# Optimization experiments

Measured on AMD Instinct MI355X. Metric: run time of the kernel, lower is better.

Reference implementation:

```python
import jax, jax.numpy as jnp
import numpy as np

B, T, FBINS = 256, 512, 128
L1, L2, L3, NCLASS = 256, 256, 128, 10
Q_SCALE = 8.0  # 4-bit fixed point in [-1, 1]


def _quant(w):
    return jnp.clip(jnp.round(w * Q_SCALE) / Q_SCALE, -1.0, 1.0)


def qw(w):
    # straight-through quantizer (identity gradient)
    return w + jax.lax.stop_gradient(_quant(w) - w)


def egru_cell(x, h, W, b, H):
    # eGRU: 2-gate cell (update gate + candidate), softsign activations
    a = jnp.concatenate([x, h], axis=-1) @ qw(W).T + b  # [B, 2H]
    z = 0.5 * (jax.nn.soft_sign(a[:, :H]) + 1.0)
    h_cand = jax.nn.soft_sign(a[:, H:])
    return z * h + (1.0 - z) * h_cand


def setup_inputs() -> dict:
    key = jax.random.key(0)
    ks = jax.random.split(key, 8)
    s = lambda fan_in: 1.0 / np.sqrt(fan_in)
    return {
        "inputs": jax.random.normal(ks[0], (B, T, FBINS), jnp.float32),
        "h1_init": jax.random.uniform(ks[1], (B, L1), jnp.float32, -1.0, 1.0),
        "h2_init": jax.random.uniform(ks[2], (B, L2), jnp.float32, -1.0, 1.0),
        "W1": jax.random.normal(ks[3], (2 * L1, FBINS + L1), jnp.float32) * s(FBINS + L1),
        "b1": jnp.zeros((2 * L1,), jnp.float32),
        "W2": jax.random.normal(ks[4], (2 * L2, L1 + L2), jnp.float32) * s(L1 + L2),
        "b2": jnp.zeros((2 * L2,), jnp.float32),
        "W3": jax.random.normal(ks[5], (L3, L2), jnp.float32) * s(L2),
        "b3": jnp.zeros((L3,), jnp.float32),
        "W4": jax.random.normal(ks[6], (NCLASS, L3), jnp.float32) * s(L3),
        "b4": jnp.zeros((NCLASS,), jnp.float32),
    }


def reference(inputs, h1_init, h2_init, W1, b1, W2, b2, W3, b3, W4, b4):
    def step(carry, x_t):
        h1, h2 = carry
        h1 = egru_cell(x_t, h1, W1, b1, L1)
        h2 = egru_cell(h1, h2, W2, b2, L2)
        h3 = jnp.maximum(h2 @ qw(W3).T + b3, 0.0)  # clamp(min=0)
        h4 = h3 @ qw(W4).T + b4
        return (h1, h2), h4

    xs = jnp.swapaxes(inputs, 0, 1)  # [T, B, F]
    _, ys = jax.lax.scan(step, (h1_init, h2_init), xs)  # [T, B, C]
    y = jnp.swapaxes(ys, 0, 1)  # [B, T, C]
    return jax.nn.log_softmax(y, axis=-1)
```

## Files before the change

### kernel.cpp

```cpp
#include <hip/hip_runtime.h>

#define NT 512
#define FB 128
#define HD 256
#define NC 10
#define NG 32
#define GR 8

typedef __attribute__((ext_vector_type(8))) short bf16x8;
typedef __attribute__((ext_vector_type(4))) float f32x4;
typedef __attribute__((ext_vector_type(4))) unsigned u32x4;

static __device__ __forceinline__ short f2bf(float f){
  union { float f; unsigned u; } v; v.f = f;
  return (short)((v.u + 0x7fffu + ((v.u >> 16) & 1u)) >> 16);
}
static __device__ __forceinline__ float bf2f(short h){
  union { unsigned u; float f; } v; v.u = ((unsigned)(unsigned short)h) << 16;
  return v.f;
}
static __device__ __forceinline__ float quantw(float w){
  return fminf(fmaxf(rintf(w * 8.0f) * 0.125f, -1.0f), 1.0f);
}
static __device__ __forceinline__ bf16x8 loadqw8(const float* __restrict__ p){
  bf16x8 v;
#pragma unroll
  for (int j = 0; j < 8; ++j) v[j] = f2bf(quantw(p[j]));
  return v;
}
static __device__ __forceinline__ void split8(f32x4 a, f32x4 b, bf16x8& hi, bf16x8& lo){
  float v0[4] = {a[0],a[1],a[2],a[3]}, v1[4] = {b[0],b[1],b[2],b[3]};
#pragma unroll
  for (int j = 0; j < 4; ++j){
    short h = f2bf(v0[j]); hi[j] = h; lo[j] = f2bf(v0[j] - bf2f(h));
  }
#pragma unroll
  for (int j = 0; j < 4; ++j){
    short h = f2bf(v1[j]); hi[4+j] = h; lo[4+j] = f2bf(v1[j] - bf2f(h));
  }
}

static __device__ __forceinline__ void st_msg(unsigned* p, short hb, short lb, unsigned ep){
  __attribute__((ext_vector_type(2))) unsigned w;
  w[0] = (((unsigned)(unsigned short)hb) << 16) | ep;
  w[1] = (((unsigned)(unsigned short)lb) << 16) | ep;
  asm volatile("global_store_dwordx2 %0, %1, off sc1" :: "v"(p), "v"(w) : "memory");
}
static __device__ __forceinline__ void gather8(const unsigned* p, unsigned ep, bf16x8& hv, bf16x8& lv){
  u32x4 a, b, c, d;
  for (;;){
    asm volatile("global_load_dwordx4 %0, %4, off sc1\n\t"
                 "global_load_dwordx4 %1, %4, off offset:16 sc1\n\t"
                 "global_load_dwordx4 %2, %4, off offset:32 sc1\n\t"
                 "global_load_dwordx4 %3, %4, off offset:48 sc1\n\t"
                 "s_waitcnt vmcnt(0)"
                 : "=&v"(a), "=&v"(b), "=&v"(c), "=&v"(d) : "v"(p) : "memory");
    unsigned m = (a[0]^ep)|(a[1]^ep)|(a[2]^ep)|(a[3]^ep)
               | (b[0]^ep)|(b[1]^ep)|(b[2]^ep)|(b[3]^ep)
               | (c[0]^ep)|(c[1]^ep)|(c[2]^ep)|(c[3]^ep)
               | (d[0]^ep)|(d[1]^ep)|(d[2]^ep)|(d[3]^ep);
    if ((m & 0xffffu) == 0u) break;
  }
  hv[0]=(short)(a[0]>>16); lv[0]=(short)(a[1]>>16);
  hv[1]=(short)(a[2]>>16); lv[1]=(short)(a[3]>>16);
  hv[2]=(short)(b[0]>>16); lv[2]=(short)(b[1]>>16);
  hv[3]=(short)(b[2]>>16); lv[3]=(short)(b[3]>>16);
  hv[4]=(short)(c[0]>>16); lv[4]=(short)(c[1]>>16);
  hv[5]=(short)(c[2]>>16); lv[5]=(short)(c[3]>>16);
  hv[6]=(short)(d[0]>>16); lv[6]=(short)(d[1]>>16);
  hv[7]=(short)(d[2]>>16); lv[7]=(short)(d[3]>>16);
}
static __device__ __forceinline__ bool chk_unpack(u32x4 a, u32x4 b, u32x4 c, u32x4 d,
                                                  unsigned ep, bf16x8& hv, bf16x8& lv){
  unsigned m = (a[0]^ep)|(a[1]^ep)|(a[2]^ep)|(a[3]^ep)
             | (b[0]^ep)|(b[1]^ep)|(b[2]^ep)|(b[3]^ep)
             | (c[0]^ep)|(c[1]^ep)|(c[2]^ep)|(c[3]^ep)
             | (d[0]^ep)|(d[1]^ep)|(d[2]^ep)|(d[3]^ep);
  if ((m & 0xffffu) != 0u) return false;
  hv[0]=(short)(a[0]>>16); lv[0]=(short)(a[1]>>16);
  hv[1]=(short)(a[2]>>16); lv[1]=(short)(a[3]>>16);
  hv[2]=(short)(b[0]>>16); lv[2]=(short)(b[1]>>16);
  hv[3]=(short)(b[2]>>16); lv[3]=(short)(b[3]>>16);
  hv[4]=(short)(c[0]>>16); lv[4]=(short)(c[1]>>16);
  hv[5]=(short)(c[2]>>16); lv[5]=(short)(c[3]>>16);
  hv[6]=(short)(d[0]>>16); lv[6]=(short)(d[1]>>16);
  hv[7]=(short)(d[2]>>16); lv[7]=(short)(d[3]>>16);
  return true;
}

#define ISSUE_G8(P,A,B,C,D) \
  asm volatile("global_load_dwordx4 %0, %4, off sc1\n\t" \
               "global_load_dwordx4 %1, %4, off offset:16 sc1\n\t" \
               "global_load_dwordx4 %2, %4, off offset:32 sc1\n\t" \
               "global_load_dwordx4 %3, %4, off offset:48 sc1" \
               : "=&v"(A),"=&v"(B),"=&v"(C),"=&v"(D) : "v"(P) : "memory")
#define ISSUE_X2(P,A,B) \
  asm volatile("global_load_dwordx4 %0, %2, off\n\t" \
               "global_load_dwordx4 %1, %2, off offset:16" \
               : "=&v"(A),"=&v"(B) : "v"(P) : "memory")
#define WAITV4(N,A,B,C,D) do{ \
  asm volatile("s_waitcnt vmcnt(" #N ")" : "+v"(A),"+v"(B),"+v"(C),"+v"(D) :: "memory"); \
  __builtin_amdgcn_sched_barrier(0); }while(0)
#define WAITV2(N,A,B) do{ \
  asm volatile("s_waitcnt vmcnt(" #N ")" : "+v"(A),"+v"(B) :: "memory"); \
  __builtin_amdgcn_sched_barrier(0); }while(0)
#define BARRIER() do{ asm volatile("s_waitcnt lgkmcnt(0)" ::: "memory"); \
  __builtin_amdgcn_s_barrier(); asm volatile("" ::: "memory"); }while(0)

__global__ __launch_bounds__(256, 1)
void egru_persistent(const float* __restrict__ xg,
                     const float* __restrict__ h1ig, const float* __restrict__ h2ig,
                     const float* __restrict__ W1g, const float* __restrict__ b1g,
                     const float* __restrict__ W2g, const float* __restrict__ b2g,
                     const float* __restrict__ W3g, const float* __restrict__ b3g,
                     const float* __restrict__ W4g, const float* __restrict__ b4g,
                     float* __restrict__ outg, float* __restrict__ wsf)
{
  const int tid = threadIdx.x;
  const int gp  = blockIdx.x & 31;
  const int sb  = blockIdx.x >> 5;
  const int wv  = tid >> 6;
  const int ln  = tid & 15;
  const int lk  = (tid >> 4) & 3;
  const int rz  = sb * 32;

  __shared__ __align__(16) short inX [16*128];
  __shared__ __align__(16) short inH1[16*256];
  __shared__ __align__(16) short inH2[16*256];
  __shared__ float aldsA[64][17];
  __shared__ float aldsB[64][17];
  __shared__ float h1own[32][GR];
  __shared__ float h2own[32][GR];
  __shared__ float h3p[128], h3q[128], h3row[128];
  __shared__ float ytmp[16];
  __shared__ float W4L[1344];
  __shared__ float b1s[64], b2s[64], b3L[128], b4L[10];

  unsigned* h1buf = reinterpret_cast<unsigned*>(wsf);
  unsigned* h2buf = h1buf + 262144;

  bf16x8 w1f[12], w2f[16], w3f[2][8];
  {
    const int arow = (wv < 2) ? (rz + wv*16 + ln) : (256 + rz + (wv-2)*16 + ln);
#pragma unroll
    for (int ks = 0; ks < 12; ++ks) w1f[ks] = loadqw8(W1g + arow*384 + ks*32 + lk*8);
#pragma unroll
    for (int ks = 0; ks < 16; ++ks) w2f[ks] = loadqw8(W2g + arow*512 + ks*32 + lk*8);
#pragma unroll
    for (int tl = 0; tl < 2; ++tl)
#pragma unroll
      for (int ks = 0; ks < 8; ++ks)
        w3f[tl][ks] = loadqw8(W3g + (wv*32 + tl*16 + ln)*256 + ks*32 + lk*8);
  }

  if (tid < 64){
    int grow = (tid < 32) ? (rz + tid) : (256 + rz + (tid - 32));
    b1s[tid] = b1g[grow];
    b2s[tid] = b2g[grow];
  }
  if (tid < 128) b3L[tid] = b3g[tid];
  if (tid < 10)  b4L[tid] = b4g[tid];
  for (int i = tid; i < 1280; i += 256){
    int c = i >> 7, k = i & 127;
    W4L[c*134 + (k>>5)*33 + (k&31)] = quantw(W4g[i]);
  }

  const int ur = tid >> 5, uc = tid & 31;
  {
    bf16x8 hv, lv;
    const float* p1 = h1ig + (size_t)(gp*GR + ur)*HD + uc*8;
    split8(*(const f32x4*)p1, *(const f32x4*)(p1+4), hv, lv);
    *(bf16x8*)((char*)inH1 + ur*512     + ((uc*16) ^ ((ur&7)<<4))) = hv;
    *(bf16x8*)((char*)inH1 + (ur+8)*512 + ((uc*16) ^ ((ur&7)<<4))) = lv;
    const float* p2 = h2ig + (size_t)(gp*GR + ur)*HD + uc*8;
    split8(*(const f32x4*)p2, *(const f32x4*)(p2+4), hv, lv);
    *(bf16x8*)((char*)inH2 + ur*512     + ((uc*16) ^ ((ur&7)<<4))) = hv;
    *(bf16x8*)((char*)inH2 + (ur+8)*512 + ((uc*16) ^ ((ur&7)<<4))) = lv;
    h1own[uc][ur] = h1ig[(size_t)(gp*GR+ur)*HD + rz + uc];
    h2own[uc][ur] = h2ig[(size_t)(gp*GR+ur)*HD + rz + uc];
  }
  const int xr = tid >> 4, xf = tid & 15;
  const int xrl = xr & 7;
  if (xr < 8){
    const float* px = xg + ((size_t)(gp*GR + xr)*NT + 0)*FB + xf*8;
    bf16x8 hv, lv;
    split8(*(const f32x4*)px, *(const f32x4*)(px+4), hv, lv);
    *(bf16x8*)((char*)inX + xr*256     + ((xf*16) ^ ((xr&7)<<4))) = hv;
    *(bf16x8*)((char*)inX + (xr+8)*256 + ((xf*16) ^ ((xr&7)<<4))) = lv;
  }
  __syncthreads();

  f32x4 acc1 = {0.f,0.f,0.f,0.f};
#pragma unroll
  for (int j = 0; j < 4; ++j){
    bf16x8 fx = *(bf16x8*)((char*)inX + ln*256 + ((j*64 + lk*16) ^ ((ln&7)<<4)));
    acc1 = __builtin_amdgcn_mfma_f32_16x16x32_bf16(w1f[j], fx, acc1, 0, 0, 0);
  }
#pragma unroll
  for (int j = 0; j < 8; ++j){
    bf16x8 fh = *(bf16x8*)((char*)inH1 + ln*512 + ((j*64 + lk*16) ^ ((ln&7)<<4)));
    acc1 = __builtin_amdgcn_mfma_f32_16x16x32_bf16(w1f[4+j], fh, acc1, 0, 0, 0);
  }

  for (int t = 0; t < NT; ++t){
    unsigned* h1s = h1buf + (unsigned)(t & 1)*131072u + (unsigned)(gp*GR)*512u;
    unsigned* h2s = h2buf + (unsigned)(t & 1)*131072u + (unsigned)(gp*GR)*512u;
    unsigned* h2r = h2buf + (unsigned)((t + 1) & 1)*131072u + (unsigned)(gp*GR)*512u;
    const bool notlast = (t + 1) < NT;

    u32x4 g2a, g2b, g2c, g2d;
    if (t > 0) ISSUE_G8(&h2r[ur*512 + uc*16], g2a, g2b, g2c, g2d);

#pragma unroll
    for (int r4 = 0; r4 < 4; ++r4)
      aldsA[wv*16 + lk*4 + r4][ln] = acc1[r4];
    BARRIER();
    {
      float az = aldsA[uc][ur]    + aldsA[uc][ur+8]    + b1s[uc];
      float ac = aldsA[32+uc][ur] + aldsA[32+uc][ur+8] + b1s[32+uc];
      float z  = 0.5f*(az/(1.0f+fabsf(az)) + 1.0f);
      float cd = ac/(1.0f+fabsf(ac));
      float hn = z*h1own[uc][ur] + (1.0f - z)*cd;
      h1own[uc][ur] = hn;
      short hb = f2bf(hn), lb = f2bf(hn - bf2f(hb));
      st_msg(&h1s[ur*512 + (rz + uc)*2], hb, lb, (unsigned)(t+1));
    }

    if (t > 0){
      WAITV4(1, g2a, g2b, g2c, g2d);
      bf16x8 hv, lv;
      if (!chk_unpack(g2a, g2b, g2c, g2d, (unsigned)t, hv, lv))
        gather8(&h2r[ur*512 + uc*16], (unsigned)t, hv, lv);
      *(bf16x8*)((char*)inH2 + ur*512     + ((uc*16) ^ ((ur&7)<<4))) = hv;
      *(bf16x8*)((char*)inH2 + (ur+8)*512 + ((uc*16) ^ ((ur&7)<<4))) = lv;
    }
    BARRIER();

    bf16x8 fh2[8];
#pragma unroll
    for (int j = 0; j < 8; ++j)
      fh2[j] = *(bf16x8*)((char*)inH2 + ln*512 + ((j*64 + lk*16) ^ ((ln&7)<<4)));
    f32x4 acc2 = {0.f,0.f,0.f,0.f};
#pragma unroll
    for (int j = 0; j < 8; ++j)
      acc2 = __builtin_amdgcn_mfma_f32_16x16x32_bf16(w2f[8+j], fh2[j], acc2, 0, 0, 0);

    u32x4 g1a, g1b, g1c, g1d;
    ISSUE_G8(&h1s[ur*512 + uc*16], g1a, g1b, g1c, g1d);
    f32x4 xa = {0,0,0,0}, xb = {0,0,0,0};
    if (notlast){
      const float* px = xg + ((size_t)(gp*GR + xrl)*NT + (t+1))*FB + xf*8;
      ISSUE_X2(px, xa, xb);
    }

    float outv = 0.f; bool dow = false; size_t oaddr = 0;
    if (t > 0){
      f32x4 acc3a = {0,0,0,0}, acc3b = {0,0,0,0};
#pragma unroll
      for (int j = 0; j < 8; ++j){
        acc3a = __builtin_amdgcn_mfma_f32_16x16x32_bf16(w3f[0][j], fh2[j], acc3a, 0, 0, 0);
        acc3b = __builtin_amdgcn_mfma_f32_16x16x32_bf16(w3f[1][j], fh2[j], acc3b, 0, 0, 0);
      }
      if (ln == sb){
#pragma unroll
        for (int r4 = 0; r4 < 4; ++r4){
          int d0 = wv*32 + lk*4 + r4;
          h3p[d0] = acc3a[r4]; h3p[d0+16] = acc3b[r4];
        }
      }
      if (ln == sb + 8){
#pragma unroll
        for (int r4 = 0; r4 < 4; ++r4){
          int d0 = wv*32 + lk*4 + r4;
          h3q[d0] = acc3a[r4]; h3q[d0+16] = acc3b[r4];
        }
      }
      BARRIER();
      if (tid < 128) h3row[tid] = fmaxf(h3p[tid] + h3q[tid] + b3L[tid], 0.0f);
      BARRIER();
      if (wv == 0){
        const int l = tid, c = l >> 2, kq = l & 3;
        float p = 0.f;
        if (c < 10){
          const float* wr = &W4L[c*134 + kq*33];
          const float* hr = &h3row[kq*32];
#pragma unroll
          for (int k = 0; k < 32; ++k) p += wr[k]*hr[k];
        }
        p += __shfl_xor(p, 1, 4);
        p += __shfl_xor(p, 2, 4);
        if (c < 10 && kq == 0) ytmp[c] = p + b4L[c];
        asm volatile("s_waitcnt lgkmcnt(0)" ::: "memory");
        float yv = (l < 10) ? ytmp[l] : -INFINITY;
        float mx = yv;
#pragma unroll
        for (int off = 1; off < 16; off <<= 1)
          mx = fmaxf(mx, __shfl_xor(mx, off, 16));
        float ex = (l < 10) ? expf(yv - mx) : 0.0f;
        float sm = ex;
#pragma unroll
        for (int off = 1; off < 16; off <<= 1)
          sm += __shfl_xor(sm, off, 16);
        if (l < 10){
          outv = yv - (mx + logf(sm));
          dow = true;
          oaddr = ((size_t)(gp*GR + sb)*NT + (t-1))*NC + l;
        }
      }
    }

    {
      if (notlast) WAITV4(2, g1a, g1b, g1c, g1d);
      else         WAITV4(0, g1a, g1b, g1c, g1d);
      bf16x8 hv, lv;
      if (!chk_unpack(g1a, g1b, g1c, g1d, (unsigned)(t+1), hv, lv))
        gather8(&h1s[ur*512 + uc*16], (unsigned)(t+1), hv, lv);
      *(bf16x8*)((char*)inH1 + ur*512     + ((uc*16) ^ ((ur&7)<<4))) = hv;
      *(bf16x8*)((char*)inH1 + (ur+8)*512 + ((uc*16) ^ ((ur&7)<<4))) = lv;
    }
    if (dow) outg[oaddr] = outv;
    BARRIER();

    bf16x8 fh1[8];
#pragma unroll
    for (int j = 0; j < 8; ++j)
      fh1[j] = *(bf16x8*)((char*)inH1 + ln*512 + ((j*64 + lk*16) ^ ((ln&7)<<4)));
#pragma unroll
    for (int j = 0; j < 8; ++j)
      acc2 = __builtin_amdgcn_mfma_f32_16x16x32_bf16(w2f[j], fh1[j], acc2, 0, 0, 0);
#pragma unroll
    for (int r4 = 0; r4 < 4; ++r4)
      aldsB[wv*16 + lk*4 + r4][ln] = acc2[r4];
    BARRIER();
    {
      float az = aldsB[uc][ur]    + aldsB[uc][ur+8]    + b2s[uc];
      float ac = aldsB[32+uc][ur] + aldsB[32+uc][ur+8] + b2s[32+uc];
      float z  = 0.5f*(az/(1.0f+fabsf(az)) + 1.0f);
      float cd = ac/(1.0f+fabsf(ac));
      float hn = z*h2own[uc][ur] + (1.0f - z)*cd;
      h2own[uc][ur] = hn;
      short hb = f2bf(hn), lb = f2bf(hn - bf2f(hb));
      st_msg(&h2s[ur*512 + (rz + uc)*2], hb, lb, (unsigned)(t+1));
    }

    if (notlast){
      WAITV2(1, xa, xb);
      if (xr < 8){
        bf16x8 hv, lv;
        split8(xa, xb, hv, lv);
        *(bf16x8*)((char*)inX + xr*256     + ((xf*16) ^ ((xr&7)<<4))) = hv;
        *(bf16x8*)((char*)inX + (xr+8)*256 + ((xf*16) ^ ((xr&7)<<4))) = lv;
      }
      BARRIER();

      f32x4 a1n = {0.f,0.f,0.f,0.f};
#pragma unroll
      for (int j = 0; j < 4; ++j){
        bf16x8 fx = *(bf16x8*)((char*)inX + ln*256 + ((j*64 + lk*16) ^ ((ln&7)<<4)));
        a1n = __builtin_amdgcn_mfma_f32_16x16x32_bf16(w1f[j], fx, a1n, 0, 0, 0);
      }
#pragma unroll
      for (int j = 0; j < 8; ++j)
        a1n = __builtin_amdgcn_mfma_f32_16x16x32_bf16(w1f[4+j], fh1[j], a1n, 0, 0, 0);
      acc1 = a1n;
    }
  }

  {
    unsigned* h2e = h2buf + (unsigned)((NT-1) & 1)*131072u + (unsigned)(gp*GR)*512u;
    bf16x8 hv, lv;
    gather8(&h2e[ur*512 + uc*16], (unsigned)NT, hv, lv);
    *(bf16x8*)((char*)inH2 + ur*512     + ((uc*16) ^ ((ur&7)<<4))) = hv;
    *(bf16x8*)((char*)inH2 + (ur+8)*512 + ((uc*16) ^ ((ur&7)<<4))) = lv;
  }
  BARRIER();
  {
    bf16x8 fh2[8];
#pragma unroll
    for (int j = 0; j < 8; ++j)
      fh2[j] = *(bf16x8*)((char*)inH2 + ln*512 + ((j*64 + lk*16) ^ ((ln&7)<<4)));
    f32x4 acc3a = {0,0,0,0}, acc3b = {0,0,0,0};
#pragma unroll
    for (int j = 0; j < 8; ++j){
      acc3a = __builtin_amdgcn_mfma_f32_16x16x32_bf16(w3f[0][j], fh2[j], acc3a, 0, 0, 0);
      acc3b = __builtin_amdgcn_mfma_f32_16x16x32_bf16(w3f[1][j], fh2[j], acc3b, 0, 0, 0);
    }
    if (ln == sb){
#pragma unroll
      for (int r4 = 0; r4 < 4; ++r4){
        int d0 = wv*32 + lk*4 + r4;
        h3p[d0] = acc3a[r4]; h3p[d0+16] = acc3b[r4];
      }
    }
    if (ln == sb + 8){
#pragma unroll
      for (int r4 = 0; r4 < 4; ++r4){
        int d0 = wv*32 + lk*4 + r4;
        h3q[d0] = acc3a[r4]; h3q[d0+16] = acc3b[r4];
      }
    }
    BARRIER();
    if (tid < 128) h3row[tid] = fmaxf(h3p[tid] + h3q[tid] + b3L[tid], 0.0f);
    BARRIER();
    if (wv == 0){
      const int l = tid, c = l >> 2, kq = l & 3;
      float p = 0.f;
      if (c < 10){
        const float* wr = &W4L[c*134 + kq*33];
        const float* hr = &h3row[kq*32];
#pragma unroll
        for (int k = 0; k < 32; ++k) p += wr[k]*hr[k];
      }
      p += __shfl_xor(p, 1, 4);
      p += __shfl_xor(p, 2, 4);
      if (c < 10 && kq == 0) ytmp[c] = p + b4L[c];
      asm volatile("s_waitcnt lgkmcnt(0)" ::: "memory");
      float yv = (l < 10) ? ytmp[l] : -INFINITY;
      float mx = yv;
#pragma unroll
      for (int off = 1; off < 16; off <<= 1)
        mx = fmaxf(mx, __shfl_xor(mx, off, 16));
      float ex = (l < 10) ? expf(yv - mx) : 0.0f;
      float sm = ex;
#pragma unroll
      for (int off = 1; off < 16; off <<= 1)
        sm += __shfl_xor(sm, off, 16);
      if (l < 10)
        outg[((size_t)(gp*GR + sb)*NT + (NT-1))*NC + l] = yv - (mx + logf(sm));
    }
  }
}

extern "C" void kernel_launch(void* const* d_in, const int* in_sizes, int n_in,
                              void* d_out, int out_size, void* d_ws, size_t ws_size,
                              hipStream_t stream) {
  const float* xg  = (const float*)d_in[0];
  const float* h1i = (const float*)d_in[1];
  const float* h2i = (const float*)d_in[2];
  const float* W1  = (const float*)d_in[3];
  const float* b1  = (const float*)d_in[4];
  const float* W2  = (const float*)d_in[5];
  const float* b2  = (const float*)d_in[6];
  const float* W3  = (const float*)d_in[7];
  const float* b3  = (const float*)d_in[8];
  const float* W4  = (const float*)d_in[9];
  const float* b4  = (const float*)d_in[10];
  float* out = (float*)d_out;
  float* ws  = (float*)d_ws;

  hipMemsetAsync(d_ws, 0, 2u * 1024u * 1024u, stream);

  egru_persistent<<<dim3(256), dim3(256), 0, stream>>>(
      xg, h1i, h2i, W1, b1, W2, b2, W3, b3, W4, b4, out, ws);
}
```

Baseline: 1.760 ms.

## Reschedule eGRU step so layer-1 update finishes early and remote loads overlap

The per-timestep loop is rotated so that the layer-1 gate update and its message store for step t+1 happen at the end of iteration t. Issue of the h2 and x global loads moves to the end of the previous iteration, so they overlap the next step's start and cross-block messages have more time to arrive before they are polled. The change also removes one barrier in the x-staging path by merging the x conversion into the h1 barrier. The risk is more subtle ordering of vmcnt waits and double-buffer indexing, which could cause stalls or correctness problems.

```diff
diff --git a/kernel.cpp b/kernel.cpp
--- a/kernel.cpp
+++ b/kernel.cpp
@@ -101,9 +101,6 @@
 #define WAITV4(N,A,B,C,D) do{ \
   asm volatile("s_waitcnt vmcnt(" #N ")" : "+v"(A),"+v"(B),"+v"(C),"+v"(D) :: "memory"); \
   __builtin_amdgcn_sched_barrier(0); }while(0)
-#define WAITV2(N,A,B) do{ \
-  asm volatile("s_waitcnt vmcnt(" #N ")" : "+v"(A),"+v"(B) :: "memory"); \
-  __builtin_amdgcn_sched_barrier(0); }while(0)
 #define BARRIER() do{ asm volatile("s_waitcnt lgkmcnt(0)" ::: "memory"); \
   __builtin_amdgcn_s_barrier(); asm volatile("" ::: "memory"); }while(0)
 
@@ -190,52 +187,58 @@
   }
   __syncthreads();
 
-  f32x4 acc1 = {0.f,0.f,0.f,0.f};
-#pragma unroll
-  for (int j = 0; j < 4; ++j){
-    bf16x8 fx = *(bf16x8*)((char*)inX + ln*256 + ((j*64 + lk*16) ^ ((ln&7)<<4)));
-    acc1 = __builtin_amdgcn_mfma_f32_16x16x32_bf16(w1f[j], fx, acc1, 0, 0, 0);
-  }
-#pragma unroll
-  for (int j = 0; j < 8; ++j){
-    bf16x8 fh = *(bf16x8*)((char*)inH1 + ln*512 + ((j*64 + lk*16) ^ ((ln&7)<<4)));
-    acc1 = __builtin_amdgcn_mfma_f32_16x16x32_bf16(w1f[4+j], fh, acc1, 0, 0, 0);
-  }
-
-  for (int t = 0; t < NT; ++t){
-    unsigned* h1s = h1buf + (unsigned)(t & 1)*131072u + (unsigned)(gp*GR)*512u;
-    unsigned* h2s = h2buf + (unsigned)(t & 1)*131072u + (unsigned)(gp*GR)*512u;
-    unsigned* h2r = h2buf + (unsigned)((t + 1) & 1)*131072u + (unsigned)(gp*GR)*512u;
-    const bool notlast = (t + 1) < NT;
-
-    u32x4 g2a, g2b, g2c, g2d;
-    if (t > 0) ISSUE_G8(&h2r[ur*512 + uc*16], g2a, g2b, g2c, g2d);
-
+  {
+    f32x4 acc1 = {0.f,0.f,0.f,0.f};
+#pragma unroll
+    for (int j = 0; j < 4; ++j){
+      bf16x8 fx = *(bf16x8*)((char*)inX + ln*256 + ((j*64 + lk*16) ^ ((ln&7)<<4)));
+      acc1 = __builtin_amdgcn_mfma_f32_16x16x32_bf16(w1f[j], fx, acc1, 0, 0, 0);
+    }
+#pragma unroll
+    for (int j = 0; j < 8; ++j){
+      bf16x8 fh = *(bf16x8*)((char*)inH1 + ln*512 + ((j*64 + lk*16) ^ ((ln&7)<<4)));
+      acc1 = __builtin_amdgcn_mfma_f32_16x16x32_bf16(w1f[4+j], fh, acc1, 0, 0, 0);
+    }
 #pragma unroll
     for (int r4 = 0; r4 < 4; ++r4)
       aldsA[wv*16 + lk*4 + r4][ln] = acc1[r4];
     BARRIER();
-    {
-      float az = aldsA[uc][ur]    + aldsA[uc][ur+8]    + b1s[uc];
-      float ac = aldsA[32+uc][ur] + aldsA[32+uc][ur+8] + b1s[32+uc];
-      float z  = 0.5f*(az/(1.0f+fabsf(az)) + 1.0f);
-      float cd = ac/(1.0f+fabsf(ac));
-      float hn = z*h1own[uc][ur] + (1.0f - z)*cd;
-      h1own[uc][ur] = hn;
-      short hb = f2bf(hn), lb = f2bf(hn - bf2f(hb));
-      st_msg(&h1s[ur*512 + (rz + uc)*2], hb, lb, (unsigned)(t+1));
-    }
+    float az = aldsA[uc][ur]    + aldsA[uc][ur+8]    + b1s[uc];
+    float ac = aldsA[32+uc][ur] + aldsA[32+uc][ur+8] + b1s[32+uc];
+    float z  = 0.5f*(az/(1.0f+fabsf(az)) + 1.0f);
+    float cd = ac/(1.0f+fabsf(ac));
+    float hn = z*h1own[uc][ur] + (1.0f - z)*cd;
+    h1own[uc][ur] = hn;
+    short hb = f2bf(hn), lb = f2bf(hn - bf2f(hb));
+    st_msg(h1buf + (unsigned)(gp*GR)*512u + ur*512 + (rz + uc)*2, hb, lb, 1u);
+  }
+  u32x4 g1a, g1b, g1c, g1d, g2a, g2b, g2c, g2d;
+  f32x4 xa = {0,0,0,0}, xb = {0,0,0,0};
+  {
+    const float* px = xg + ((size_t)(gp*GR + xrl)*NT + 1)*FB + xf*8;
+    ISSUE_X2(px, xa, xb);
+  }
+  ISSUE_G8(h1buf + (unsigned)(gp*GR)*512u + ur*512 + uc*16, g1a, g1b, g1c, g1d);
+
+  for (int t = 0; t < NT; ++t){
+    unsigned* h1r = h1buf + (unsigned)(t & 1)*131072u + (unsigned)(gp*GR)*512u;
+    unsigned* h1w = h1buf + (unsigned)((t+1) & 1)*131072u + (unsigned)(gp*GR)*512u;
+    unsigned* h2w = h2buf + (unsigned)(t & 1)*131072u + (unsigned)(gp*GR)*512u;
+    unsigned* h2r = h2buf + (unsigned)((t + 1) & 1)*131072u + (unsigned)(gp*GR)*512u;
+    const bool haveX = (t + 1) < NT;
 
     if (t > 0){
-      WAITV4(1, g2a, g2b, g2c, g2d);
+      if (t < NT-1) WAITV4(2, g2a, g2b, g2c, g2d);
+      else          WAITV4(0, g2a, g2b, g2c, g2d);
       bf16x8 hv, lv;
       if (!chk_unpack(g2a, g2b, g2c, g2d, (unsigned)t, hv, lv))
         gather8(&h2r[ur*512 + uc*16], (unsigned)t, hv, lv);
       *(bf16x8*)((char*)inH2 + ur*512     + ((uc*16) ^ ((ur&7)<<4))) = hv;
       *(bf16x8*)((char*)inH2 + (ur+8)*512 + ((uc*16) ^ ((ur&7)<<4))) = lv;
-    }
-    BARRIER();
-
+      BARRIER();
+    }
+
+    if (t > 0) ISSUE_G8(&h1r[ur*512 + uc*16], g1a, g1b, g1c, g1d);
     bf16x8 fh2[8];
 #pragma unroll
     for (int j = 0; j < 8; ++j)
@@ -244,14 +247,6 @@
 #pragma unroll
     for (int j = 0; j < 8; ++j)
       acc2 = __builtin_amdgcn_mfma_f32_16x16x32_bf16(w2f[8+j], fh2[j], acc2, 0, 0, 0);
-
-    u32x4 g1a, g1b, g1c, g1d;
-    ISSUE_G8(&h1s[ur*512 + uc*16], g1a, g1b, g1c, g1d);
-    f32x4 xa = {0,0,0,0}, xb = {0,0,0,0};
-    if (notlast){
-      const float* px = xg + ((size_t)(gp*GR + xrl)*NT + (t+1))*FB + xf*8;
-      ISSUE_X2(px, xa, xb);
-    }
 
     float outv = 0.f; bool dow = false; size_t oaddr = 0;
     if (t > 0){
@@ -309,16 +304,20 @@
       }
     }
 
+    WAITV4(0, g1a, g1b, g1c, g1d);
     {
-      if (notlast) WAITV4(2, g1a, g1b, g1c, g1d);
-      else         WAITV4(0, g1a, g1b, g1c, g1d);
       bf16x8 hv, lv;
       if (!chk_unpack(g1a, g1b, g1c, g1d, (unsigned)(t+1), hv, lv))
-        gather8(&h1s[ur*512 + uc*16], (unsigned)(t+1), hv, lv);
+        gather8(&h1r[ur*512 + uc*16], (unsigned)(t+1), hv, lv);
       *(bf16x8*)((char*)inH1 + ur*512     + ((uc*16) ^ ((ur&7)<<4))) = hv;
       *(bf16x8*)((char*)inH1 + (ur+8)*512 + ((uc*16) ^ ((ur&7)<<4))) = lv;
     }
-    if (dow) outg[oaddr] = outv;
+    if (haveX && xr < 8){
+      bf16x8 hv, lv;
+      split8(xa, xb, hv, lv);
+      *(bf16x8*)((char*)inX + xr*256     + ((xf*16) ^ ((xr&7)<<4))) = hv;
+      *(bf16x8*)((char*)inX + (xr+8)*256 + ((xf*16) ^ ((xr&7)<<4))) = lv;
+    }
     BARRIER();
 
     bf16x8 fh1[8];
@@ -340,29 +339,38 @@
       float hn = z*h2own[uc][ur] + (1.0f - z)*cd;
       h2own[uc][ur] = hn;
       short hb = f2bf(hn), lb = f2bf(hn - bf2f(hb));
-      st_msg(&h2s[ur*512 + (rz + uc)*2], hb, lb, (unsigned)(t+1));
-    }
-
-    if (notlast){
-      WAITV2(1, xa, xb);
-      if (xr < 8){
-        bf16x8 hv, lv;
-        split8(xa, xb, hv, lv);
-        *(bf16x8*)((char*)inX + xr*256     + ((xf*16) ^ ((xr&7)<<4))) = hv;
-        *(bf16x8*)((char*)inX + (xr+8)*256 + ((xf*16) ^ ((xr&7)<<4))) = lv;
-      }
-      BARRIER();
-
-      f32x4 a1n = {0.f,0.f,0.f,0.f};
+      st_msg(&h2w[ur*512 + (rz + uc)*2], hb, lb, (unsigned)(t+1));
+    }
+
+    if (haveX){
+      f32x4 acc1 = {0.f,0.f,0.f,0.f};
 #pragma unroll
       for (int j = 0; j < 4; ++j){
         bf16x8 fx = *(bf16x8*)((char*)inX + ln*256 + ((j*64 + lk*16) ^ ((ln&7)<<4)));
-        a1n = __builtin_amdgcn_mfma_f32_16x16x32_bf16(w1f[j], fx, a1n, 0, 0, 0);
+        acc1 = __builtin_amdgcn_mfma_f32_16x16x32_bf16(w1f[j], fx, acc1, 0, 0, 0);
       }
 #pragma unroll
       for (int j = 0; j < 8; ++j)
-        a1n = __builtin_amdgcn_mfma_f32_16x16x32_bf16(w1f[4+j], fh1[j], a1n, 0, 0, 0);
-      acc1 = a1n;
+        acc1 = __builtin_amdgcn_mfma_f32_16x16x32_bf16(w1f[4+j], fh1[j], acc1, 0, 0, 0);
+#pragma unroll
+      for (int r4 = 0; r4 < 4; ++r4)
+        aldsA[wv*16 + lk*4 + r4][ln] = acc1[r4];
+      BARRIER();
+      float az = aldsA[uc][ur]    + aldsA[uc][ur+8]    + b1s[uc];
+      float ac = aldsA[32+uc][ur] + aldsA[32+uc][ur+8] + b1s[32+uc];
+      float z  = 0.5f*(az/(1.0f+fabsf(az)) + 1.0f);
+      float cd = ac/(1.0f+fabsf(ac));
+      float hn = z*h1own[uc][ur] + (1.0f - z)*cd;
+      h1own[uc][ur] = hn;
+      short hb = f2bf(hn), lb = f2bf(hn - bf2f(hb));
+      st_msg(&h1w[ur*512 + (rz + uc)*2], hb, lb, (unsigned)(t+2));
+    }
+
+    if (dow) outg[oaddr] = outv;
+    if (t < NT-1) ISSUE_G8(&h2w[ur*512 + uc*16], g2a, g2b, g2c, g2d);
+    if (t + 2 < NT){
+      const float* px = xg + ((size_t)(gp*GR + xrl)*NT + (t+2))*FB + xf*8;
+      ISSUE_X2(px, xa, xb);
     }
   }
 
```

Result: slower. 2.220 ms (+26.1%).

## Split each group's batch rows into two independent MFMA streams and prefetch earlier

Applied to the files above, without the earlier changes.

Each workgroup now processes two half-groups of 4 batch rows (rows gp*4 and 128+gp*4) as two independent accumulator chains A and B. The two chains interleave their MFMA dependency sequences, which is meant to hide MFMA latency on the serial recurrence. The h2 exchange load and the next-step x load are issued at the end of the previous iteration, so the wait shifts from the start of the step to the end. The costs are zero-padded LDS tiles (half the MFMA columns are wasted), doubled LDS, and more registers for the fragments.

```diff
diff --git a/kernel.cpp b/kernel.cpp
--- a/kernel.cpp
+++ b/kernel.cpp
@@ -4,8 +4,6 @@
 #define FB 128
 #define HD 256
 #define NC 10
-#define NG 32
-#define GR 8
 
 typedef __attribute__((ext_vector_type(8))) short bf16x8;
 typedef __attribute__((ext_vector_type(4))) float f32x4;
@@ -101,9 +99,6 @@
 #define WAITV4(N,A,B,C,D) do{ \
   asm volatile("s_waitcnt vmcnt(" #N ")" : "+v"(A),"+v"(B),"+v"(C),"+v"(D) :: "memory"); \
   __builtin_amdgcn_sched_barrier(0); }while(0)
-#define WAITV2(N,A,B) do{ \
-  asm volatile("s_waitcnt vmcnt(" #N ")" : "+v"(A),"+v"(B) :: "memory"); \
-  __builtin_amdgcn_sched_barrier(0); }while(0)
 #define BARRIER() do{ asm volatile("s_waitcnt lgkmcnt(0)" ::: "memory"); \
   __builtin_amdgcn_s_barrier(); asm volatile("" ::: "memory"); }while(0)
 
@@ -124,13 +119,21 @@
   const int lk  = (tid >> 4) & 3;
   const int rz  = sb * 32;
 
-  __shared__ __align__(16) short inX [16*128];
-  __shared__ __align__(16) short inH1[16*256];
-  __shared__ __align__(16) short inH2[16*256];
-  __shared__ float aldsA[64][17];
-  __shared__ float aldsB[64][17];
-  __shared__ float h1own[32][GR];
-  __shared__ float h2own[32][GR];
+  const int rc  = tid >> 7;
+  const int th  = tid & 127;
+  const int r_  = th >> 5;
+  const int d_  = th & 31;
+  const int grow = rc*128 + gp*4 + r_;
+  const int xr  = th >> 4, xf = th & 15;
+  const int xrow = rc*128 + gp*4 + (xr & 3);
+
+  __shared__ __align__(16) short inX [2*16*128];
+  __shared__ __align__(16) short inH1[2*16*256];
+  __shared__ __align__(16) short inH2[2*16*256];
+  __shared__ float alds1[2][64][17];
+  __shared__ float alds2[2][64][17];
+  __shared__ float h1own[2][32][4];
+  __shared__ float h2own[2][32][4];
   __shared__ float h3p[128], h3q[128], h3row[128];
   __shared__ float ytmp[16];
   __shared__ float W4L[1344];
@@ -154,9 +157,9 @@
   }
 
   if (tid < 64){
-    int grow = (tid < 32) ? (rz + tid) : (256 + rz + (tid - 32));
-    b1s[tid] = b1g[grow];
-    b2s[tid] = b2g[grow];
+    int grw = (tid < 32) ? (rz + tid) : (256 + rz + (tid - 32));
+    b1s[tid] = b1g[grw];
+    b2s[tid] = b2g[grw];
   }
   if (tid < 128) b3L[tid] = b3g[tid];
   if (tid < 10)  b4L[tid] = b4g[tid];
@@ -165,114 +168,134 @@
     W4L[c*134 + (k>>5)*33 + (k&31)] = quantw(W4g[i]);
   }
 
-  const int ur = tid >> 5, uc = tid & 31;
+  for (int i = tid; i < 2048; i += 256) ((int*)inX )[i] = 0;
+  for (int i = tid; i < 4096; i += 256) ((int*)inH1)[i] = 0;
+  for (int i = tid; i < 4096; i += 256) ((int*)inH2)[i] = 0;
+  __syncthreads();
+
   {
     bf16x8 hv, lv;
-    const float* p1 = h1ig + (size_t)(gp*GR + ur)*HD + uc*8;
+    const float* p1 = h1ig + (size_t)grow*HD + d_*8;
     split8(*(const f32x4*)p1, *(const f32x4*)(p1+4), hv, lv);
-    *(bf16x8*)((char*)inH1 + ur*512     + ((uc*16) ^ ((ur&7)<<4))) = hv;
-    *(bf16x8*)((char*)inH1 + (ur+8)*512 + ((uc*16) ^ ((ur&7)<<4))) = lv;
-    const float* p2 = h2ig + (size_t)(gp*GR + ur)*HD + uc*8;
+    char* bH1 = (char*)inH1 + rc*8192;
+    *(bf16x8*)(bH1 + r_*512     + ((d_*16) ^ ((r_&7)<<4))) = hv;
+    *(bf16x8*)(bH1 + (r_+8)*512 + ((d_*16) ^ ((r_&7)<<4))) = lv;
+    const float* p2 = h2ig + (size_t)grow*HD + d_*8;
     split8(*(const f32x4*)p2, *(const f32x4*)(p2+4), hv, lv);
-    *(bf16x8*)((char*)inH2 + ur*512     + ((uc*16) ^ ((ur&7)<<4))) = hv;
-    *(bf16x8*)((char*)inH2 + (ur+8)*512 + ((uc*16) ^ ((ur&7)<<4))) = lv;
-    h1own[uc][ur] = h1ig[(size_t)(gp*GR+ur)*HD + rz + uc];
-    h2own[uc][ur] = h2ig[(size_t)(gp*GR+ur)*HD + rz + uc];
-  }
-  const int xr = tid >> 4, xf = tid & 15;
-  const int xrl = xr & 7;
-  if (xr < 8){
-    const float* px = xg + ((size_t)(gp*GR + xr)*NT + 0)*FB + xf*8;
+    char* bH2 = (char*)inH2 + rc*8192;
+    *(bf16x8*)(bH2 + r_*512     + ((d_*16) ^ ((r_&7)<<4))) = hv;
+    *(bf16x8*)(bH2 + (r_+8)*512 + ((d_*16) ^ ((r_&7)<<4))) = lv;
+    h1own[rc][d_][r_] = h1ig[(size_t)grow*HD + rz + d_];
+    h2own[rc][d_][r_] = h2ig[(size_t)grow*HD + rz + d_];
+  }
+  if (xr < 4){
+    const float* px = xg + ((size_t)(rc*128 + gp*4 + xr)*NT + 0)*FB + xf*8;
     bf16x8 hv, lv;
     split8(*(const f32x4*)px, *(const f32x4*)(px+4), hv, lv);
-    *(bf16x8*)((char*)inX + xr*256     + ((xf*16) ^ ((xr&7)<<4))) = hv;
-    *(bf16x8*)((char*)inX + (xr+8)*256 + ((xf*16) ^ ((xr&7)<<4))) = lv;
+    char* bX = (char*)inX + rc*4096;
+    *(bf16x8*)(bX + xr*256     + ((xf*16) ^ (xr<<4))) = hv;
+    *(bf16x8*)(bX + (xr+8)*256 + ((xf*16) ^ (xr<<4))) = lv;
   }
   __syncthreads();
 
-  f32x4 acc1 = {0.f,0.f,0.f,0.f};
+  f32x4 accA = {0.f,0.f,0.f,0.f}, accB = {0.f,0.f,0.f,0.f};
 #pragma unroll
   for (int j = 0; j < 4; ++j){
-    bf16x8 fx = *(bf16x8*)((char*)inX + ln*256 + ((j*64 + lk*16) ^ ((ln&7)<<4)));
-    acc1 = __builtin_amdgcn_mfma_f32_16x16x32_bf16(w1f[j], fx, acc1, 0, 0, 0);
+    bf16x8 fxA = *(bf16x8*)((char*)inX + 0    + ln*256 + ((j*64 + lk*16) ^ ((ln&7)<<4)));
+    bf16x8 fxB = *(bf16x8*)((char*)inX + 4096 + ln*256 + ((j*64 + lk*16) ^ ((ln&7)<<4)));
+    accA = __builtin_amdgcn_mfma_f32_16x16x32_bf16(w1f[j], fxA, accA, 0, 0, 0);
+    accB = __builtin_amdgcn_mfma_f32_16x16x32_bf16(w1f[j], fxB, accB, 0, 0, 0);
   }
 #pragma unroll
   for (int j = 0; j < 8; ++j){
-    bf16x8 fh = *(bf16x8*)((char*)inH1 + ln*512 + ((j*64 + lk*16) ^ ((ln&7)<<4)));
-    acc1 = __builtin_amdgcn_mfma_f32_16x16x32_bf16(w1f[4+j], fh, acc1, 0, 0, 0);
-  }
+    bf16x8 fhA = *(bf16x8*)((char*)inH1 + 0    + ln*512 + ((j*64 + lk*16) ^ ((ln&7)<<4)));
+    bf16x8 fhB = *(bf16x8*)((char*)inH1 + 8192 + ln*512 + ((j*64 + lk*16) ^ ((ln&7)<<4)));
+    accA = __builtin_amdgcn_mfma_f32_16x16x32_bf16(w1f[4+j], fhA, accA, 0, 0, 0);
+    accB = __builtin_amdgcn_mfma_f32_16x16x32_bf16(w1f[4+j], fhB, accB, 0, 0, 0);
+  }
+  f32x4 xa = {0,0,0,0}, xb = {0,0,0,0};
+  ISSUE_X2(xg + ((size_t)xrow*NT + 1)*FB + xf*8, xa, xb);
+  u32x4 g1a, g1b, g1c, g1d, g2a, g2b, g2c, g2d;
 
   for (int t = 0; t < NT; ++t){
-    unsigned* h1s = h1buf + (unsigned)(t & 1)*131072u + (unsigned)(gp*GR)*512u;
-    unsigned* h2s = h2buf + (unsigned)(t & 1)*131072u + (unsigned)(gp*GR)*512u;
-    unsigned* h2r = h2buf + (unsigned)((t + 1) & 1)*131072u + (unsigned)(gp*GR)*512u;
+    unsigned* h1s = h1buf + (unsigned)(t & 1)*131072u;
+    unsigned* h2s = h2buf + (unsigned)(t & 1)*131072u;
+    unsigned* h2r = h2buf + (unsigned)((t + 1) & 1)*131072u;
     const bool notlast = (t + 1) < NT;
 
-    u32x4 g2a, g2b, g2c, g2d;
-    if (t > 0) ISSUE_G8(&h2r[ur*512 + uc*16], g2a, g2b, g2c, g2d);
-
-#pragma unroll
-    for (int r4 = 0; r4 < 4; ++r4)
-      aldsA[wv*16 + lk*4 + r4][ln] = acc1[r4];
+#pragma unroll
+    for (int r4 = 0; r4 < 4; ++r4){
+      alds1[0][wv*16 + lk*4 + r4][ln] = accA[r4];
+      alds1[1][wv*16 + lk*4 + r4][ln] = accB[r4];
+    }
     BARRIER();
     {
-      float az = aldsA[uc][ur]    + aldsA[uc][ur+8]    + b1s[uc];
-      float ac = aldsA[32+uc][ur] + aldsA[32+uc][ur+8] + b1s[32+uc];
+      float az = alds1[rc][d_][r_]    + alds1[rc][d_][r_+8]    + b1s[d_];
+      float ac = alds1[rc][32+d_][r_] + alds1[rc][32+d_][r_+8] + b1s[32+d_];
       float z  = 0.5f*(az/(1.0f+fabsf(az)) + 1.0f);
       float cd = ac/(1.0f+fabsf(ac));
-      float hn = z*h1own[uc][ur] + (1.0f - z)*cd;
-      h1own[uc][ur] = hn;
+      float hn = z*h1own[rc][d_][r_] + (1.0f - z)*cd;
+      h1own[rc][d_][r_] = hn;
       short hb = f2bf(hn), lb = f2bf(hn - bf2f(hb));
-      st_msg(&h1s[ur*512 + (rz + uc)*2], hb, lb, (unsigned)(t+1));
+      st_msg(h1s + (unsigned)grow*512u + (rz + d_)*2, hb, lb, (unsigned)(t+1));
     }
 
     if (t > 0){
-      WAITV4(1, g2a, g2b, g2c, g2d);
+      WAITV4(3, g2a, g2b, g2c, g2d);
       bf16x8 hv, lv;
       if (!chk_unpack(g2a, g2b, g2c, g2d, (unsigned)t, hv, lv))
-        gather8(&h2r[ur*512 + uc*16], (unsigned)t, hv, lv);
-      *(bf16x8*)((char*)inH2 + ur*512     + ((uc*16) ^ ((ur&7)<<4))) = hv;
-      *(bf16x8*)((char*)inH2 + (ur+8)*512 + ((uc*16) ^ ((ur&7)<<4))) = lv;
+        gather8(h2r + (unsigned)grow*512u + d_*16, (unsigned)t, hv, lv);
+      char* bH2 = (char*)inH2 + rc*8192;
+      *(bf16x8*)(bH2 + r_*512     + ((d_*16) ^ ((r_&7)<<4))) = hv;
+      *(bf16x8*)(bH2 + (r_+8)*512 + ((d_*16) ^ ((r_&7)<<4))) = lv;
     }
     BARRIER();
 
-    bf16x8 fh2[8];
+    bf16x8 fh2A[8], fh2B[8];
+#pragma unroll
+    for (int j = 0; j < 8; ++j){
+      fh2A[j] = *(bf16x8*)((char*)inH2 + 0    + ln*512 + ((j*64 + lk*16) ^ ((ln&7)<<4)));
+      fh2B[j] = *(bf16x8*)((char*)inH2 + 8192 + ln*512 + ((j*64 + lk*16) ^ ((ln&7)<<4)));
+    }
+    f32x4 ac2A = {0.f,0.f,0.f,0.f}, ac2B = {0.f,0.f,0.f,0.f};
 #pragma unroll
     for (int j = 0; j < 8; ++j)
-      fh2[j] = *(bf16x8*)((char*)inH2 + ln*512 + ((j*64 + lk*16) ^ ((ln&7)<<4)));
-    f32x4 acc2 = {0.f,0.f,0.f,0.f};
+      ac2A = __builtin_amdgcn_mfma_f32_16x16x32_bf16(w2f[8+j], fh2A[j], ac2A, 0, 0, 0);
 #pragma unroll
     for (int j = 0; j < 8; ++j)
-      acc2 = __builtin_amdgcn_mfma_f32_16x16x32_bf16(w2f[8+j], fh2[j], acc2, 0, 0, 0);
-
-    u32x4 g1a, g1b, g1c, g1d;
-    ISSUE_G8(&h1s[ur*512 + uc*16], g1a, g1b, g1c, g1d);
-    f32x4 xa = {0,0,0,0}, xb = {0,0,0,0};
-    if (notlast){
-      const float* px = xg + ((size_t)(gp*GR + xrl)*NT + (t+1))*FB + xf*8;
-      ISSUE_X2(px, xa, xb);
-    }
+      ac2B = __builtin_amdgcn_mfma_f32_16x16x32_bf16(w2f[8+j], fh2B[j], ac2B, 0, 0, 0);
+
+    ISSUE_G8(h1s + (unsigned)grow*512u + d_*16, g1a, g1b, g1c, g1d);
 
     float outv = 0.f; bool dow = false; size_t oaddr = 0;
     if (t > 0){
-      f32x4 acc3a = {0,0,0,0}, acc3b = {0,0,0,0};
-#pragma unroll
-      for (int j = 0; j < 8; ++j){
-        acc3a = __builtin_amdgcn_mfma_f32_16x16x32_bf16(w3f[0][j], fh2[j], acc3a, 0, 0, 0);
-        acc3b = __builtin_amdgcn_mfma_f32_16x16x32_bf16(w3f[1][j], fh2[j], acc3b, 0, 0, 0);
-      }
-      if (ln == sb){
+      const int hcol = sb & 3;
+      f32x4 a3a = {0,0,0,0}, a3b = {0,0,0,0};
+      if (sb < 4){
+#pragma unroll
+        for (int j = 0; j < 8; ++j){
+          a3a = __builtin_amdgcn_mfma_f32_16x16x32_bf16(w3f[0][j], fh2A[j], a3a, 0, 0, 0);
+          a3b = __builtin_amdgcn_mfma_f32_16x16x32_bf16(w3f[1][j], fh2A[j], a3b, 0, 0, 0);
+        }
+      } else {
+#pragma unroll
+        for (int j = 0; j < 8; ++j){
+          a3a = __builtin_amdgcn_mfma_f32_16x16x32_bf16(w3f[0][j], fh2B[j], a3a, 0, 0, 0);
+          a3b = __builtin_amdgcn_mfma_f32_16x16x32_bf16(w3f[1][j], fh2B[j], a3b, 0, 0, 0);
+        }
+      }
+      if (ln == hcol){
 #pragma unroll
         for (int r4 = 0; r4 < 4; ++r4){
           int d0 = wv*32 + lk*4 + r4;
-          h3p[d0] = acc3a[r4]; h3p[d0+16] = acc3b[r4];
+          h3p[d0] = a3a[r4]; h3p[d0+16] = a3b[r4];
         }
       }
-      if (ln == sb + 8){
+      if (ln == hcol + 8){
 #pragma unroll
         for (int r4 = 0; r4 < 4; ++r4){
           int d0 = wv*32 + lk*4 + r4;
-          h3q[d0] = acc3a[r4]; h3q[d0+16] = acc3b[r4];
+          h3q[d0] = a3a[r4]; h3q[d0+16] = a3b[r4];
         }
       }
       BARRIER();
@@ -302,101 +325,122 @@
         for (int off = 1; off < 16; off <<= 1)
           sm += __shfl_xor(sm, off, 16);
         if (l < 10){
+          int orow = (sb < 4) ? (gp*4 + sb) : (128 + gp*4 + (sb - 4));
           outv = yv - (mx + logf(sm));
           dow = true;
-          oaddr = ((size_t)(gp*GR + sb)*NT + (t-1))*NC + l;
+          oaddr = ((size_t)orow*NT + (t-1))*NC + l;
         }
       }
     }
 
+    WAITV4(0, g1a, g1b, g1c, g1d);
     {
-      if (notlast) WAITV4(2, g1a, g1b, g1c, g1d);
-      else         WAITV4(0, g1a, g1b, g1c, g1d);
       bf16x8 hv, lv;
       if (!chk_unpack(g1a, g1b, g1c, g1d, (unsigned)(t+1), hv, lv))
-        gather8(&h1s[ur*512 + uc*16], (unsigned)(t+1), hv, lv);
-      *(bf16x8*)((char*)inH1 + ur*512     + ((uc*16) ^ ((ur&7)<<4))) = hv;
-      *(bf16x8*)((char*)inH1 + (ur+8)*512 + ((uc*16) ^ ((ur&7)<<4))) = lv;
-    }
-    if (dow) outg[oaddr] = outv;
+        gather8(h1s + (unsigned)grow*512u + d_*16, (unsigned)(t+1), hv, lv);
+      char* bH1 = (char*)inH1 + rc*8192;
+      *(bf16x8*)(bH1 + r_*512     + ((d_*16) ^ ((r_&7)<<4))) = hv;
+      *(bf16x8*)(bH1 + (r_+8)*512 + ((d_*16) ^ ((r_&7)<<4))) = lv;
+    }
+    if (notlast && xr < 4){
+      bf16x8 hv, lv;
+      split8(xa, xb, hv, lv);
+      char* bX = (char*)inX + rc*4096;
+      *(bf16x8*)(bX + xr*256     + ((xf*16) ^ (xr<<4))) = hv;
+      *(bf16x8*)(bX + (xr+8)*256 + ((xf*16) ^ (xr<<4))) = lv;
+    }
     BARRIER();
 
-    bf16x8 fh1[8];
+    bf16x8 fh1A[8], fh1B[8];
+#pragma unroll
+    for (int j = 0; j < 8; ++j){
+      fh1A[j] = *(bf16x8*)((char*)inH1 + 0    + ln*512 + ((j*64 + lk*16) ^ ((ln&7)<<4)));
+      fh1B[j] = *(bf16x8*)((char*)inH1 + 8192 + ln*512 + ((j*64 + lk*16) ^ ((ln&7)<<4)));
+    }
 #pragma unroll
     for (int j = 0; j < 8; ++j)
-      fh1[j] = *(bf16x8*)((char*)inH1 + ln*512 + ((j*64 + lk*16) ^ ((ln&7)<<4)));
+      ac2A = __builtin_amdgcn_mfma_f32_16x16x32_bf16(w2f[j], fh1A[j], ac2A, 0, 0, 0);
 #pragma unroll
     for (int j = 0; j < 8; ++j)
-      acc2 = __builtin_amdgcn_mfma_f32_16x16x32_bf16(w2f[j], fh1[j], acc2, 0, 0, 0);
-#pragma unroll
-    for (int r4 = 0; r4 < 4; ++r4)
-      aldsB[wv*16 + lk*4 + r4][ln] = acc2[r4];
+      ac2B = __builtin_amdgcn_mfma_f32_16x16x32_bf16(w2f[j], fh1B[j], ac2B, 0, 0, 0);
+#pragma unroll
+    for (int r4 = 0; r4 < 4; ++r4){
+      alds2[0][wv*16 + lk*4 + r4][ln] = ac2A[r4];
+      alds2[1][wv*16 + lk*4 + r4][ln] = ac2B[r4];
+    }
     BARRIER();
     {
-      float az = aldsB[uc][ur]    + aldsB[uc][ur+8]    + b2s[uc];
-      float ac = aldsB[32+uc][ur] + aldsB[32+uc][ur+8] + b2s[32+uc];
+      float az = alds2[rc][d_][r_]    + alds2[rc][d_][r_+8]    + b2s[d_];
+      float ac = alds2[rc][32+d_][r_] + alds2[rc][32+d_][r_+8] + b2s[32+d_];
       float z  = 0.5f*(az/(1.0f+fabsf(az)) + 1.0f);
       float cd = ac/(1.0f+fabsf(ac));
-      float hn = z*h2own[uc][ur] + (1.0f - z)*cd;
-      h2own[uc][ur] = hn;
+      float hn = z*h2own[rc][d_][r_] + (1.0f - z)*cd;
+      h2own[rc][d_][r_] = hn;
       short hb = f2bf(hn), lb = f2bf(hn - bf2f(hb));
-      st_msg(&h2s[ur*512 + (rz + uc)*2], hb, lb, (unsigned)(t+1));
+      st_msg(h2s + (unsigned)grow*512u + (rz + d_)*2, hb, lb, (unsigned)(t+1));
     }
 
     if (notlast){
-      WAITV2(1, xa, xb);
-      if (xr < 8){
-        bf16x8 hv, lv;
-        split8(xa, xb, hv, lv);
-        *(bf16x8*)((char*)inX + xr*256     + ((xf*16) ^ ((xr&7)<<4))) = hv;
-        *(bf16x8*)((char*)inX + (xr+8)*256 + ((xf*16) ^ ((xr&7)<<4))) = lv;
-      }
-      BARRIER();
-
-      f32x4 a1n = {0.f,0.f,0.f,0.f};
+      f32x4 nA = {0.f,0.f,0.f,0.f}, nB = {0.f,0.f,0.f,0.f};
 #pragma unroll
       for (int j = 0; j < 4; ++j){
-        bf16x8 fx = *(bf16x8*)((char*)inX + ln*256 + ((j*64 + lk*16) ^ ((ln&7)<<4)));
-        a1n = __builtin_amdgcn_mfma_f32_16x16x32_bf16(w1f[j], fx, a1n, 0, 0, 0);
-      }
-#pragma unroll
-      for (int j = 0; j < 8; ++j)
-        a1n = __builtin_amdgcn_mfma_f32_16x16x32_bf16(w1f[4+j], fh1[j], a1n, 0, 0, 0);
-      acc1 = a1n;
-    }
+        bf16x8 fxA = *(bf16x8*)((char*)inX + 0    + ln*256 + ((j*64 + lk*16) ^ ((ln&7)<<4)));
+        bf16x8 fxB = *(bf16x8*)((char*)inX + 4096 + ln*256 + ((j*64 + lk*16) ^ ((ln&7)<<4)));
+        nA = __builtin_amdgcn_mfma_f32_16x16x32_bf16(w1f[j], fxA, nA, 0, 0, 0);
+        nB = __builtin_amdgcn_mfma_f32_16x16x32_bf16(w1f[j], fxB, nB, 0, 0, 0);
+      }
+#pragma unroll
+      for (int j = 0; j < 8; ++j){
+        nA = __builtin_amdgcn_mfma_f32_16x16x32_bf16(w1f[4+j], fh1A[j], nA, 0, 0, 0);
+        nB = __builtin_amdgcn_mfma_f32_16x16x32_bf16(w1f[4+j], fh1B[j], nB, 0, 0, 0);
+      }
+      accA = nA; accB = nB;
+    }
+
+    ISSUE_G8(h2s + (unsigned)grow*512u + d_*16, g2a, g2b, g2c, g2d);
+    {
+      int xt = (t + 2 < NT) ? (t + 2) : (NT - 1);
+      ISSUE_X2(xg + ((size_t)xrow*NT + xt)*FB + xf*8, xa, xb);
+    }
+    if (dow) outg[oaddr] = outv;
   }
 
   {
-    unsigned* h2e = h2buf + (unsigned)((NT-1) & 1)*131072u + (unsigned)(gp*GR)*512u;
+    unsigned* h2e = h2buf + (unsigned)((NT-1) & 1)*131072u;
+    WAITV4(0, g2a, g2b, g2c, g2d);
     bf16x8 hv, lv;
-    gather8(&h2e[ur*512 + uc*16], (unsigned)NT, hv, lv);
-    *(bf16x8*)((char*)inH2 + ur*512     + ((uc*16) ^ ((ur&7)<<4))) = hv;
-    *(bf16x8*)((char*)inH2 + (ur+8)*512 + ((uc*16) ^ ((ur&7)<<4))) = lv;
+    if (!chk_unpack(g2a, g2b, g2c, g2d, (unsigned)NT, hv, lv))
+      gather8(h2e + (unsigned)grow*512u + d_*16, (unsigned)NT, hv, lv);
+    char* bH2 = (char*)inH2 + rc*8192;
+    *(bf16x8*)(bH2 + r_*512     + ((d_*16) ^ ((r_&7)<<4))) = hv;
+    *(bf16x8*)(bH2 + (r_+8)*512 + ((d_*16) ^ ((r_&7)<<4))) = lv;
   }
   BARRIER();
   {
-    bf16x8 fh2[8];
+    const int hcol = sb & 3;
+    const int hoff = (sb < 4) ? 0 : 8192;
+    bf16x8 fhh[8];
 #pragma unroll
     for (int j = 0; j < 8; ++j)
-      fh2[j] = *(bf16x8*)((char*)inH2 + ln*512 + ((j*64 + lk*16) ^ ((ln&7)<<4)));
-    f32x4 acc3a = {0,0,0,0}, acc3b = {0,0,0,0};
+      fhh[j] = *(bf16x8*)((char*)inH2 + hoff + ln*512 + ((j*64 + lk*16) ^ ((ln&7)<<4)));
+    f32x4 a3a = {0,0,0,0}, a3b = {0,0,0,0};
 #pragma unroll
     for (int j = 0; j < 8; ++j){
-      acc3a = __builtin_amdgcn_mfma_f32_16x16x32_bf16(w3f[0][j], fh2[j], acc3a, 0, 0, 0);
-      acc3b = __builtin_amdgcn_mfma_f32_16x16x32_bf16(w3f[1][j], fh2[j], acc3b, 0, 0, 0);
-    }
-    if (ln == sb){
+      a3a = __builtin_amdgcn_mfma_f32_16x16x32_bf16(w3f[0][j], fhh[j], a3a, 0, 0, 0);
+      a3b = __builtin_amdgcn_mfma_f32_16x16x32_bf16(w3f[1][j], fhh[j], a3b, 0, 0, 0);
+    }
+    if (ln == hcol){
 #pragma unroll
       for (int r4 = 0; r4 < 4; ++r4){
         int d0 = wv*32 + lk*4 + r4;
-        h3p[d0] = acc3a[r4]; h3p[d0+16] = acc3b[r4];
-      }
-    }
-    if (ln == sb + 8){
+        h3p[d0] = a3a[r4]; h3p[d0+16] = a3b[r4];
+      }
+    }
+    if (ln == hcol + 8){
 #pragma unroll
       for (int r4 = 0; r4 < 4; ++r4){
         int d0 = wv*32 + lk*4 + r4;
-        h3q[d0] = acc3a[r4]; h3q[d0+16] = acc3b[r4];
+        h3q[d0] = a3a[r4]; h3q[d0+16] = a3b[r4];
       }
     }
     BARRIER();
@@ -425,8 +469,10 @@
 #pragma unroll
       for (int off = 1; off < 16; off <<= 1)
         sm += __shfl_xor(sm, off, 16);
-      if (l < 10)
-        outg[((size_t)(gp*GR + sb)*NT + (NT-1))*NC + l] = yv - (mx + logf(sm));
+      if (l < 10){
+        int orow = (sb < 4) ? (gp*4 + sb) : (128 + gp*4 + (sb - 4));
+        outg[((size_t)orow*NT + (NT-1))*NC + l] = yv - (mx + logf(sm));
+      }
     }
   }
 }
```

Result: slower. 2.015 ms (+14.5%).
